# Performance work log

Hardware: AMD Instinct MI355X
Metric: run time of the kernel (lower is better)

## Reference

```python
import jax, jax.numpy as jnp
import numpy as np

N_ENT = 40000
D = 128
B = 1024
EPS = 1e-7  # BCE clamp for numerical stability (torch clamps logs internally)


def _cdist_euclidean(a, e):
    # a: [B, D], e: [N, D] -> [B, N] via GEMM-based squared-distance expansion
    sq = jnp.sum(a * a, axis=1)[:, None] + jnp.sum(e * e, axis=1)[None, :] - 2.0 * (a @ e.T)
    return jnp.sqrt(jnp.maximum(sq, 0.0))


def _cdist_manhattan(a, e):
    # Sequential over batch rows to avoid materializing [B, N, D]
    return jax.lax.map(lambda row: jnp.sum(jnp.abs(row[None, :] - e), axis=1), a)


def _branch_loss(c, ent, t_idx, l1_flag, positive):
    dist = _cdist_manhattan(c, ent) if l1_flag else _cdist_euclidean(c, ent)
    # original Python double-loop: dist[i][j] = 1/dist[i][j] * 100
    scaled = 100.0 / jnp.maximum(dist, 1e-12)
    pred = jnp.clip(jax.nn.sigmoid(scaled), EPS, 1.0 - EPS)
    if positive:
        y = jnp.zeros_like(pred).at[jnp.arange(pred.shape[0]), t_idx].set(1.0)
        bce = y * jnp.log(pred) + (1.0 - y) * jnp.log(1.0 - pred)
    else:
        # negative branch writes 0 into an all-zeros target -> y == 0
        bce = jnp.log(1.0 - pred)
    return -jnp.mean(bce)


def setup_inputs() -> dict:
    key = jax.random.key(0)
    ks = jax.random.split(key, 7)
    return {
        "pos_h_batch": jax.random.randint(ks[0], (B,), 0, N_ENT),
        "pos_t_batch": jax.random.randint(ks[1], (B,), 0, N_ENT),
        "neg_h_batch": jax.random.randint(ks[2], (B,), 0, N_ENT),
        "neg_t_batch": jax.random.randint(ks[3], (B,), 0, N_ENT),
        "rseq_pos": jax.random.normal(ks[4], (B, D), jnp.float32),
        "rseq_neg": jax.random.normal(ks[5], (B, D), jnp.float32),
        "ent_embeddings": jax.random.normal(ks[6], (N_ENT, D), jnp.float32),
        "L1_flag": 0,
    }


def reference(pos_h_batch, pos_t_batch, neg_h_batch, neg_t_batch, rseq_pos, rseq_neg, ent_embeddings, L1_flag):
    l1 = bool(L1_flag)
    # positive branch
    c_t_pos = ent_embeddings[pos_h_batch] + rseq_pos
    loss1 = _branch_loss(c_t_pos, ent_embeddings, pos_t_batch, l1, positive=True)
    # negative branch (neg_t_batch only feeds an unused c_h_e in the original)
    c_t_neg = ent_embeddings[neg_h_batch] + rseq_neg
    loss2 = _branch_loss(c_t_neg, ent_embeddings, None, l1, positive=False)
    return loss1 + loss2
```

## Files before the change

kernel.cpp:

```cpp
#include <hip/hip_runtime.h>
#include <cstdint>
#include <cstddef>

#define N_ENT 40000
#define DDIM  128
#define BSZ   1024
#define NJT   313
#define NPART (16 * NJT)
#define NGRID 5120

#define AS1 __attribute__((address_space(1)))
#define AS3 __attribute__((address_space(3)))

typedef short s16x8 __attribute__((ext_vector_type(8)));
typedef float f32x4 __attribute__((ext_vector_type(4)));

#define OFF_PART  0
#define OFF_TPART 20480
#define OFF_ENORM 24576
#define OFF_CNORM 184576
#define OFF_CBF   192768
#define OFF_EBF   717056

#define S_CLAMP 15.9423847f
#define U_CLAMP 0.159423847f
#define LP_MAX (-1.1920929e-7f)

__device__ __forceinline__ unsigned short f2bf(float f) {
  uint32_t u = __float_as_uint(f);
  u += 0x7fffu + ((u >> 16) & 1u);
  return (unsigned short)(u >> 16);
}

__global__ __launch_bounds__(256) void prep_k(const float* __restrict__ ent,
                                              const int* __restrict__ pos_h,
                                              const int* __restrict__ pos_t,
                                              const int* __restrict__ neg_h,
                                              const float* __restrict__ rpos,
                                              const float* __restrict__ rneg,
                                              const int* __restrict__ l1_flag,
                                              unsigned short* __restrict__ ent_bf,
                                              float* __restrict__ enorm,
                                              unsigned short* __restrict__ c_bf,
                                              float* __restrict__ cnorm,
                                              float* __restrict__ tpart) {
  const int lane = threadIdx.x & 63, wv = threadIdx.x >> 6;
  const int ih = lane >> 5, il = lane & 31;
  const int blk = blockIdx.x;
  if (blk < 5000) {
    int row = blk * 8 + wv * 2 + ih;
    float4 v = reinterpret_cast<const float4*>(ent + (size_t)row * DDIM)[il];
    ushort4 h4; h4.x = f2bf(v.x); h4.y = f2bf(v.y); h4.z = f2bf(v.z); h4.w = f2bf(v.w);
    reinterpret_cast<ushort4*>(ent_bf + (size_t)row * DDIM)[il] = h4;
    float sq = fmaf(v.x, v.x, fmaf(v.y, v.y, fmaf(v.z, v.z, v.w * v.w)));
    #pragma unroll
    for (int m = 1; m <= 16; m <<= 1) sq += __shfl_xor(sq, m);
    if (il == 0) enorm[row] = sq;
  } else {
    int row = (blk - 5000) * 8 + wv * 2 + ih;
    int br = row >> 10, i = row & 1023;
    int h = br ? neg_h[i] : pos_h[i];
    const float* rs = br ? rneg : rpos;
    float4 e  = reinterpret_cast<const float4*>(ent + (size_t)h * DDIM)[il];
    float4 rv = reinterpret_cast<const float4*>(rs + (size_t)i * DDIM)[il];
    float c0 = e.x + rv.x, c1 = e.y + rv.y, c2 = e.z + rv.z, c3 = e.w + rv.w;
    ushort4 h4; h4.x = f2bf(c0); h4.y = f2bf(c1); h4.z = f2bf(c2); h4.w = f2bf(c3);
    reinterpret_cast<ushort4*>(c_bf + (size_t)row * DDIM)[il] = h4;
    float sq = fmaf(c0, c0, fmaf(c1, c1, fmaf(c2, c2, c3 * c3)));
    #pragma unroll
    for (int m = 1; m <= 16; m <<= 1) sq += __shfl_xor(sq, m);
    if (il == 0) cnorm[row] = sq;
    if (br == 0) {
      int t = pos_t[i];
      float4 et = reinterpret_cast<const float4*>(ent + (size_t)t * DDIM)[il];
      float d0 = c0 - et.x, d1 = c1 - et.y, d2v = c2 - et.z, d3 = c3 - et.w;
      float d2 = fmaf(d0, d0, fmaf(d1, d1, fmaf(d2v, d2v, d3 * d3)));
      float m1 = fabsf(d0) + fabsf(d1) + fabsf(d2v) + fabsf(d3);
      #pragma unroll
      for (int m = 1; m <= 16; m <<= 1) { d2 += __shfl_xor(d2, m); m1 += __shfl_xor(m1, m); }
      if (il == 0) {
        float s = (*l1_flag) ? (100.f / fmaxf(m1, 1e-12f))
                             : (100.f * rsqrtf(fmaxf(d2, 0.f)));
        float x  = __expf(-s);
        float L  = log1pf(x);
        float Bt = fminf(-L, LP_MAX);
        float Ap = fmaxf(-s, -S_CLAMP);
        tpart[i] = Bt - Ap;
      }
    }
  }
}

__global__ __launch_bounds__(256) void main_k(const unsigned short* __restrict__ c_bf,
                                              const unsigned short* __restrict__ ent_bf,
                                              const float* __restrict__ cnorm,
                                              const float* __restrict__ enorm,
                                              const int* __restrict__ l1_flag,
                                              const int* __restrict__ pos_h,
                                              const int* __restrict__ neg_h,
                                              const float* __restrict__ rpos,
                                              const float* __restrict__ rneg,
                                              const float* __restrict__ ent_f32,
                                              float* __restrict__ partials) {
  __shared__ unsigned short smem[128 * 128];
  const int id = blockIdx.x;
  const int c8 = id & 7;
  const int q  = id >> 3;
  const int tg = q >> 4;
  const int mm = q & 15;
  const int jt = c8 + tg * 8;
  if (jt >= NJT) return;
  const int branch = mm & 1;
  const int it = mm >> 1;
  const int i0 = it * 128, j0 = jt * 128;
  const int tid = threadIdx.x, lane = tid & 63, wv = tid >> 6;
  const int wm = wv >> 1, wn = wv & 1;
  const int r15 = lane & 15, quad = lane >> 4;

  #pragma unroll
  for (int i = 0; i < 8; ++i) {
    int g  = i * 256 + tid;
    int r  = g >> 4;
    int cp = g & 15;
    int c  = cp ^ (r & 15);
    int jr = j0 + r; if (jr >= N_ENT) jr = N_ENT - 1;
    const unsigned short* src = ent_bf + (size_t)jr * DDIM + c * 8;
    __builtin_amdgcn_global_load_lds((const AS1 void*)src, (AS3 void*)(&smem[g * 8]), 16, 0, 0);
  }

  const unsigned short* Abase = c_bf + ((size_t)(branch << 10) + i0) * DDIM;
  const unsigned short* arow[4];
  #pragma unroll
  for (int tm = 0; tm < 4; ++tm)
    arow[tm] = Abase + (size_t)(wm * 64 + tm * 16 + r15) * DDIM + quad * 8;

  s16x8 av[2][4];
  #pragma unroll
  for (int tm = 0; tm < 4; ++tm)
    av[0][tm] = *reinterpret_cast<const s16x8*>(arow[tm]);

  float en[4];
  #pragma unroll
  for (int tn = 0; tn < 4; ++tn) {
    int jg = j0 + wn * 64 + tn * 16 + r15;
    en[tn] = enorm[jg < N_ENT ? jg : N_ENT - 1];
  }
  float cnv[16];
  #pragma unroll
  for (int tm = 0; tm < 4; ++tm)
    #pragma unroll
    for (int r = 0; r < 4; ++r)
      cnv[tm * 4 + r] = cnorm[(branch << 10) + i0 + wm * 64 + tm * 16 + quad * 4 + r];

  f32x4 acc[4][4];
  const f32x4 zf = {0.f, 0.f, 0.f, 0.f};
  #pragma unroll
  for (int a = 0; a < 4; ++a)
    #pragma unroll
    for (int b = 0; b < 4; ++b) acc[a][b] = zf;

  __syncthreads();

  #pragma unroll
  for (int kc = 0; kc < 4; ++kc) {
    if (kc < 3) {
      #pragma unroll
      for (int tm = 0; tm < 4; ++tm)
        av[(kc + 1) & 1][tm] = *reinterpret_cast<const s16x8*>(arow[tm] + (kc + 1) * 32);
    }
    s16x8 bv[4];
    #pragma unroll
    for (int tn = 0; tn < 4; ++tn) {
      int R  = wn * 64 + tn * 16 + r15;
      int cs = (kc * 4 + quad) ^ r15;
      bv[tn] = *reinterpret_cast<const s16x8*>(&smem[R * 128 + cs * 8]);
    }
    #pragma unroll
    for (int tm = 0; tm < 4; ++tm)
      #pragma unroll
      for (int tn = 0; tn < 4; ++tn)
        acc[tm][tn] = __builtin_amdgcn_mfma_f32_16x16x32_bf16(av[kc & 1][tm], bv[tn], acc[tm][tn], 0, 0, 0);
  }

  const int l1 = *l1_flag;
  float ls0 = 0.f, ls1 = 0.f, ls2 = 0.f, ls3 = 0.f;
  const bool full = (j0 + 128) <= N_ENT;

  if (!l1) {
    #pragma unroll
    for (int tm = 0; tm < 4; ++tm) {
      if (full) {
        #pragma unroll
        for (int tn = 0; tn < 4; ++tn) {
          float e0 = en[tn];
          float u0 = rsqrtf(fmaf(-2.f, acc[tm][tn][0], cnv[tm * 4 + 0] + e0));
          float u1 = rsqrtf(fmaf(-2.f, acc[tm][tn][1], cnv[tm * 4 + 1] + e0));
          float u2 = rsqrtf(fmaf(-2.f, acc[tm][tn][2], cnv[tm * 4 + 2] + e0));
          float u3 = rsqrtf(fmaf(-2.f, acc[tm][tn][3], cnv[tm * 4 + 3] + e0));
          ls0 += fminf(u0, U_CLAMP);
          ls1 += fminf(u1, U_CLAMP);
          ls2 += fminf(u2, U_CLAMP);
          ls3 += fminf(u3, U_CLAMP);
        }
      } else {
        #pragma unroll
        for (int tn = 0; tn < 4; ++tn) {
          int jg = j0 + wn * 64 + tn * 16 + r15;
          if (jg < N_ENT) {
            float e0 = en[tn];
            ls0 += fminf(rsqrtf(fmaf(-2.f, acc[tm][tn][0], cnv[tm * 4 + 0] + e0)), U_CLAMP);
            ls1 += fminf(rsqrtf(fmaf(-2.f, acc[tm][tn][1], cnv[tm * 4 + 1] + e0)), U_CLAMP);
            ls2 += fminf(rsqrtf(fmaf(-2.f, acc[tm][tn][2], cnv[tm * 4 + 2] + e0)), U_CLAMP);
            ls3 += fminf(rsqrtf(fmaf(-2.f, acc[tm][tn][3], cnv[tm * 4 + 3] + e0)), U_CLAMP);
          }
        }
      }
    }
  } else {
    const float* rs = branch ? rneg : rpos;
    const int*   hb = branch ? neg_h : pos_h;
    #pragma unroll 1
    for (int tm = 0; tm < 4; ++tm) {
      #pragma unroll 1
      for (int r = 0; r < 4; ++r) {
        int bi = i0 + wm * 64 + tm * 16 + quad * 4 + r;
        int h  = hb[bi];
        #pragma unroll 1
        for (int tn = 0; tn < 4; ++tn) {
          int jg = j0 + wn * 64 + tn * 16 + r15;
          if (jg < N_ENT) {
            const float* cp1 = ent_f32 + (size_t)h * DDIM;
            const float* cp2 = rs + (size_t)bi * DDIM;
            const float* ep  = ent_f32 + (size_t)jg * DDIM;
            float man = 0.f;
            #pragma unroll 1
            for (int d = 0; d < DDIM; ++d) man += fabsf(cp1[d] + cp2[d] - ep[d]);
            float s = 100.f / fmaxf(man, 1e-12f);
            ls0 += 0.01f * fminf(s, S_CLAMP);
          }
        }
      }
    }
  }
  float lsum = (ls0 + ls1) + (ls2 + ls3);

  #pragma unroll
  for (int m = 32; m; m >>= 1) lsum += __shfl_xor(lsum, m);
  __shared__ float s4[4];
  if (lane == 0) s4[wv] = lsum;
  __syncthreads();
  if (tid == 0)
    partials[jt * 16 + mm] = s4[0] + s4[1] + s4[2] + s4[3];
}

__global__ __launch_bounds__(256) void finalize_k(const float* __restrict__ partials,
                                                  const float* __restrict__ tpart,
                                                  float* __restrict__ out) {
  const int b = blockIdx.x, tid = threadIdx.x, lane = tid & 63, wv = tid >> 6;
  const double inv = 1.0 / ((double)BSZ * (double)N_ENT);
  double v = 0.0;
  if (b < 20) {
    int i = b * 256 + tid;
    if (i < NPART) v = (double)partials[i] * (100.0 * inv);
  } else {
    int i = (b - 20) * 256 + tid;
    v = (double)tpart[i] * (-inv);
  }
  #pragma unroll
  for (int m = 32; m; m >>= 1) v += __shfl_xor(v, m);
  __shared__ double sd[4];
  if (lane == 0) sd[wv] = v;
  __syncthreads();
  if (tid == 0) atomicAdd(out, (float)(sd[0] + sd[1] + sd[2] + sd[3]));
}

extern "C" void kernel_launch(void* const* d_in, const int* in_sizes, int n_in,
                              void* d_out, int out_size, void* d_ws, size_t ws_size,
                              hipStream_t stream) {
  const int*   pos_h = (const int*)d_in[0];
  const int*   pos_t = (const int*)d_in[1];
  const int*   neg_h = (const int*)d_in[2];
  const float* rpos  = (const float*)d_in[4];
  const float* rneg  = (const float*)d_in[5];
  const float* ent   = (const float*)d_in[6];
  const int*   l1    = (const int*)d_in[7];

  char* ws = (char*)d_ws;
  float*          partials = (float*)(ws + OFF_PART);
  float*          tpart    = (float*)(ws + OFF_TPART);
  float*          enorm    = (float*)(ws + OFF_ENORM);
  float*          cnorm    = (float*)(ws + OFF_CNORM);
  unsigned short* c_bf     = (unsigned short*)(ws + OFF_CBF);
  unsigned short* ent_bf   = (unsigned short*)(ws + OFF_EBF);

  hipMemsetAsync(d_out, 0, sizeof(float), stream);

  prep_k<<<5256, 256, 0, stream>>>(ent, pos_h, pos_t, neg_h, rpos, rneg, l1,
                                   ent_bf, enorm, c_bf, cnorm, tpart);

  main_k<<<NGRID, 256, 0, stream>>>(c_bf, ent_bf, cnorm, enorm, l1,
                                    pos_h, neg_h, rpos, rneg, ent, partials);

  finalize_k<<<24, 256, 0, stream>>>(partials, tpart, (float*)d_out);
}
```

Measured before the change: 144.2 us.

## Reuse each staged entity tile across four row tiles per block and single-block finalize

Each main_k block now loads one 128-entity bf16 tile into LDS once and loops over four consecutive row tiles (branch/i0 pairs), cutting the grid from 5120 to 1280 blocks and reducing redundant LDS staging of the entity tile by 4x. The next row tile's A fragments and norms are prefetched while the current tile's epilogue runs. The finalize kernel becomes a single 1024-thread block that writes the output directly, removing the memset and the atomics. The trade-off is fewer blocks available to hide latency and a serialized inner loop per block.

```diff
diff --git a/kernel.cpp b/kernel.cpp
--- a/kernel.cpp
+++ b/kernel.cpp
@@ -7,7 +7,7 @@
 #define BSZ   1024
 #define NJT   313
 #define NPART (16 * NJT)
-#define NGRID 5120
+#define NGRID 1280
 
 #define AS1 __attribute__((address_space(1)))
 #define AS3 __attribute__((address_space(3)))
@@ -103,16 +103,15 @@
                                               const float* __restrict__ ent_f32,
                                               float* __restrict__ partials) {
   __shared__ unsigned short smem[128 * 128];
+  __shared__ float s4[4][4];
   const int id = blockIdx.x;
   const int c8 = id & 7;
   const int q  = id >> 3;
-  const int tg = q >> 4;
-  const int mm = q & 15;
+  const int tg = q >> 2;
+  const int h  = q & 3;
   const int jt = c8 + tg * 8;
   if (jt >= NJT) return;
-  const int branch = mm & 1;
-  const int it = mm >> 1;
-  const int i0 = it * 128, j0 = jt * 128;
+  const int j0 = jt * 128;
   const int tid = threadIdx.x, lane = tid & 63, wv = tid >> 6;
   const int wm = wv >> 1, wn = wv & 1;
   const int r15 = lane & 15, quad = lane >> 4;
@@ -128,16 +127,31 @@
     __builtin_amdgcn_global_load_lds((const AS1 void*)src, (AS3 void*)(&smem[g * 8]), 16, 0, 0);
   }
 
-  const unsigned short* Abase = c_bf + ((size_t)(branch << 10) + i0) * DDIM;
+#define SET_AROW(mm_) do {                                                     \
+    int b_ = (mm_) & 1, i0_ = ((mm_) >> 1) * 128;                              \
+    const unsigned short* Ab = c_bf + ((size_t)(b_ << 10) + i0_) * DDIM;       \
+    _Pragma("unroll")                                                          \
+    for (int tm = 0; tm < 4; ++tm)                                             \
+      arow[tm] = Ab + (size_t)(wm * 64 + tm * 16 + r15) * DDIM + quad * 8;     \
+  } while (0)
+
+#define LOAD_CNV(mm_) do {                                                     \
+    int b_ = (mm_) & 1, i0_ = ((mm_) >> 1) * 128;                              \
+    _Pragma("unroll")                                                          \
+    for (int tm = 0; tm < 4; ++tm)                                             \
+      _Pragma("unroll")                                                        \
+      for (int r = 0; r < 4; ++r)                                              \
+        cnvA[tm * 4 + r] = cnorm[(b_ << 10) + i0_ + wm * 64 + tm * 16 + quad * 4 + r]; \
+  } while (0)
+
   const unsigned short* arow[4];
-  #pragma unroll
-  for (int tm = 0; tm < 4; ++tm)
-    arow[tm] = Abase + (size_t)(wm * 64 + tm * 16 + r15) * DDIM + quad * 8;
-
   s16x8 av[2][4];
+  float cnvA[16];
+  SET_AROW(h * 4);
   #pragma unroll
   for (int tm = 0; tm < 4; ++tm)
     av[0][tm] = *reinterpret_cast<const s16x8*>(arow[tm]);
+  LOAD_CNV(h * 4);
 
   float en[4];
   #pragma unroll
@@ -145,133 +159,145 @@
     int jg = j0 + wn * 64 + tn * 16 + r15;
     en[tn] = enorm[jg < N_ENT ? jg : N_ENT - 1];
   }
-  float cnv[16];
-  #pragma unroll
-  for (int tm = 0; tm < 4; ++tm)
-    #pragma unroll
-    for (int r = 0; r < 4; ++r)
-      cnv[tm * 4 + r] = cnorm[(branch << 10) + i0 + wm * 64 + tm * 16 + quad * 4 + r];
-
-  f32x4 acc[4][4];
+
+  const int l1 = *l1_flag;
+  const bool full = (j0 + 128) <= N_ENT;
   const f32x4 zf = {0.f, 0.f, 0.f, 0.f};
-  #pragma unroll
-  for (int a = 0; a < 4; ++a)
-    #pragma unroll
-    for (int b = 0; b < 4; ++b) acc[a][b] = zf;
 
   __syncthreads();
 
-  #pragma unroll
-  for (int kc = 0; kc < 4; ++kc) {
-    if (kc < 3) {
+  #pragma unroll 1
+  for (int k = 0; k < 4; ++k) {
+    const int mm = h * 4 + k;
+    const int branch = mm & 1;
+    const int i0 = (mm >> 1) * 128;
+
+    f32x4 acc[4][4];
+    #pragma unroll
+    for (int a = 0; a < 4; ++a)
+      #pragma unroll
+      for (int b = 0; b < 4; ++b) acc[a][b] = zf;
+
+    #pragma unroll
+    for (int kc = 0; kc < 4; ++kc) {
+      if (kc < 3) {
+        #pragma unroll
+        for (int tm = 0; tm < 4; ++tm)
+          av[(kc + 1) & 1][tm] = *reinterpret_cast<const s16x8*>(arow[tm] + (kc + 1) * 32);
+      }
+      s16x8 bv[4];
+      #pragma unroll
+      for (int tn = 0; tn < 4; ++tn) {
+        int R  = wn * 64 + tn * 16 + r15;
+        int cs = (kc * 4 + quad) ^ r15;
+        bv[tn] = *reinterpret_cast<const s16x8*>(&smem[R * 128 + cs * 8]);
+      }
       #pragma unroll
       for (int tm = 0; tm < 4; ++tm)
-        av[(kc + 1) & 1][tm] = *reinterpret_cast<const s16x8*>(arow[tm] + (kc + 1) * 32);
+        #pragma unroll
+        for (int tn = 0; tn < 4; ++tn)
+          acc[tm][tn] = __builtin_amdgcn_mfma_f32_16x16x32_bf16(av[kc & 1][tm], bv[tn], acc[tm][tn], 0, 0, 0);
     }
-    s16x8 bv[4];
-    #pragma unroll
-    for (int tn = 0; tn < 4; ++tn) {
-      int R  = wn * 64 + tn * 16 + r15;
-      int cs = (kc * 4 + quad) ^ r15;
-      bv[tn] = *reinterpret_cast<const s16x8*>(&smem[R * 128 + cs * 8]);
+
+    if (k < 3) {
+      SET_AROW(mm + 1);
+      #pragma unroll
+      for (int tm = 0; tm < 4; ++tm)
+        av[0][tm] = *reinterpret_cast<const s16x8*>(arow[tm]);
     }
-    #pragma unroll
-    for (int tm = 0; tm < 4; ++tm)
-      #pragma unroll
-      for (int tn = 0; tn < 4; ++tn)
-        acc[tm][tn] = __builtin_amdgcn_mfma_f32_16x16x32_bf16(av[kc & 1][tm], bv[tn], acc[tm][tn], 0, 0, 0);
-  }
-
-  const int l1 = *l1_flag;
-  float ls0 = 0.f, ls1 = 0.f, ls2 = 0.f, ls3 = 0.f;
-  const bool full = (j0 + 128) <= N_ENT;
-
-  if (!l1) {
-    #pragma unroll
-    for (int tm = 0; tm < 4; ++tm) {
-      if (full) {
-        #pragma unroll
-        for (int tn = 0; tn < 4; ++tn) {
-          float e0 = en[tn];
-          float u0 = rsqrtf(fmaf(-2.f, acc[tm][tn][0], cnv[tm * 4 + 0] + e0));
-          float u1 = rsqrtf(fmaf(-2.f, acc[tm][tn][1], cnv[tm * 4 + 1] + e0));
-          float u2 = rsqrtf(fmaf(-2.f, acc[tm][tn][2], cnv[tm * 4 + 2] + e0));
-          float u3 = rsqrtf(fmaf(-2.f, acc[tm][tn][3], cnv[tm * 4 + 3] + e0));
-          ls0 += fminf(u0, U_CLAMP);
-          ls1 += fminf(u1, U_CLAMP);
-          ls2 += fminf(u2, U_CLAMP);
-          ls3 += fminf(u3, U_CLAMP);
-        }
-      } else {
-        #pragma unroll
-        for (int tn = 0; tn < 4; ++tn) {
-          int jg = j0 + wn * 64 + tn * 16 + r15;
-          if (jg < N_ENT) {
+
+    float ls0 = 0.f, ls1 = 0.f, ls2 = 0.f, ls3 = 0.f;
+    if (!l1) {
+      #pragma unroll
+      for (int tm = 0; tm < 4; ++tm) {
+        if (full) {
+          #pragma unroll
+          for (int tn = 0; tn < 4; ++tn) {
             float e0 = en[tn];
-            ls0 += fminf(rsqrtf(fmaf(-2.f, acc[tm][tn][0], cnv[tm * 4 + 0] + e0)), U_CLAMP);
-            ls1 += fminf(rsqrtf(fmaf(-2.f, acc[tm][tn][1], cnv[tm * 4 + 1] + e0)), U_CLAMP);
-            ls2 += fminf(rsqrtf(fmaf(-2.f, acc[tm][tn][2], cnv[tm * 4 + 2] + e0)), U_CLAMP);
-            ls3 += fminf(rsqrtf(fmaf(-2.f, acc[tm][tn][3], cnv[tm * 4 + 3] + e0)), U_CLAMP);
+            float u0 = rsqrtf(fmaf(-2.f, acc[tm][tn][0], cnvA[tm * 4 + 0] + e0));
+            float u1 = rsqrtf(fmaf(-2.f, acc[tm][tn][1], cnvA[tm * 4 + 1] + e0));
+            float u2 = rsqrtf(fmaf(-2.f, acc[tm][tn][2], cnvA[tm * 4 + 2] + e0));
+            float u3 = rsqrtf(fmaf(-2.f, acc[tm][tn][3], cnvA[tm * 4 + 3] + e0));
+            ls0 += fminf(u0, U_CLAMP);
+            ls1 += fminf(u1, U_CLAMP);
+            ls2 += fminf(u2, U_CLAMP);
+            ls3 += fminf(u3, U_CLAMP);
+          }
+        } else {
+          #pragma unroll
+          for (int tn = 0; tn < 4; ++tn) {
+            int jg = j0 + wn * 64 + tn * 16 + r15;
+            if (jg < N_ENT) {
+              float e0 = en[tn];
+              ls0 += fminf(rsqrtf(fmaf(-2.f, acc[tm][tn][0], cnvA[tm * 4 + 0] + e0)), U_CLAMP);
+              ls1 += fminf(rsqrtf(fmaf(-2.f, acc[tm][tn][1], cnvA[tm * 4 + 1] + e0)), U_CLAMP);
+              ls2 += fminf(rsqrtf(fmaf(-2.f, acc[tm][tn][2], cnvA[tm * 4 + 2] + e0)), U_CLAMP);
+              ls3 += fminf(rsqrtf(fmaf(-2.f, acc[tm][tn][3], cnvA[tm * 4 + 3] + e0)), U_CLAMP);
+            }
           }
         }
       }
-    }
-  } else {
-    const float* rs = branch ? rneg : rpos;
-    const int*   hb = branch ? neg_h : pos_h;
-    #pragma unroll 1
-    for (int tm = 0; tm < 4; ++tm) {
+    } else {
+      const float* rs = branch ? rneg : rpos;
+      const int*   hb = branch ? neg_h : pos_h;
       #pragma unroll 1
-      for (int r = 0; r < 4; ++r) {
-        int bi = i0 + wm * 64 + tm * 16 + quad * 4 + r;
-        int h  = hb[bi];
+      for (int tm = 0; tm < 4; ++tm) {
         #pragma unroll 1
-        for (int tn = 0; tn < 4; ++tn) {
-          int jg = j0 + wn * 64 + tn * 16 + r15;
-          if (jg < N_ENT) {
-            const float* cp1 = ent_f32 + (size_t)h * DDIM;
-            const float* cp2 = rs + (size_t)bi * DDIM;
-            const float* ep  = ent_f32 + (size_t)jg * DDIM;
-            float man = 0.f;
-            #pragma unroll 1
-            for (int d = 0; d < DDIM; ++d) man += fabsf(cp1[d] + cp2[d] - ep[d]);
-            float s = 100.f / fmaxf(man, 1e-12f);
-            ls0 += 0.01f * fminf(s, S_CLAMP);
+        for (int r = 0; r < 4; ++r) {
+          int bi = i0 + wm * 64 + tm * 16 + quad * 4 + r;
+          int hh = hb[bi];
+          #pragma unroll 1
+          for (int tn = 0; tn < 4; ++tn) {
+            int jg = j0 + wn * 64 + tn * 16 + r15;
+            if (jg < N_ENT) {
+              const float* cp1 = ent_f32 + (size_t)hh * DDIM;
+              const float* cp2 = rs + (size_t)bi * DDIM;
+              const float* ep  = ent_f32 + (size_t)jg * DDIM;
+              float man = 0.f;
+              #pragma unroll 1
+              for (int d = 0; d < DDIM; ++d) man += fabsf(cp1[d] + cp2[d] - ep[d]);
+              float s = 100.f / fmaxf(man, 1e-12f);
+              ls0 += 0.01f * fminf(s, S_CLAMP);
+            }
           }
         }
       }
     }
-  }
-  float lsum = (ls0 + ls1) + (ls2 + ls3);
-
-  #pragma unroll
-  for (int m = 32; m; m >>= 1) lsum += __shfl_xor(lsum, m);
-  __shared__ float s4[4];
-  if (lane == 0) s4[wv] = lsum;
+    float lsum = (ls0 + ls1) + (ls2 + ls3);
+
+    #pragma unroll
+    for (int m = 32; m; m >>= 1) lsum += __shfl_xor(lsum, m);
+    if (lane == 0) s4[k][wv] = lsum;
+
+    if (k < 3) LOAD_CNV(mm + 1);
+  }
+
   __syncthreads();
-  if (tid == 0)
-    partials[jt * 16 + mm] = s4[0] + s4[1] + s4[2] + s4[3];
-}
-
-__global__ __launch_bounds__(256) void finalize_k(const float* __restrict__ partials,
-                                                  const float* __restrict__ tpart,
-                                                  float* __restrict__ out) {
-  const int b = blockIdx.x, tid = threadIdx.x, lane = tid & 63, wv = tid >> 6;
+  if (tid < 4)
+    partials[jt * 16 + h * 4 + tid] = s4[tid][0] + s4[tid][1] + s4[tid][2] + s4[tid][3];
+#undef SET_AROW
+#undef LOAD_CNV
+}
+
+__global__ __launch_bounds__(1024) void finalize_k(const float* __restrict__ partials,
+                                                   const float* __restrict__ tpart,
+                                                   float* __restrict__ out) {
+  const int tid = threadIdx.x, lane = tid & 63, wv = tid >> 6;
   const double inv = 1.0 / ((double)BSZ * (double)N_ENT);
   double v = 0.0;
-  if (b < 20) {
-    int i = b * 256 + tid;
-    if (i < NPART) v = (double)partials[i] * (100.0 * inv);
-  } else {
-    int i = (b - 20) * 256 + tid;
-    v = (double)tpart[i] * (-inv);
-  }
+  for (int i = tid; i < NPART; i += 1024) v += (double)partials[i] * (100.0 * inv);
+  v += (double)tpart[tid] * (-inv);
   #pragma unroll
   for (int m = 32; m; m >>= 1) v += __shfl_xor(v, m);
-  __shared__ double sd[4];
+  __shared__ double sd[16];
   if (lane == 0) sd[wv] = v;
   __syncthreads();
-  if (tid == 0) atomicAdd(out, (float)(sd[0] + sd[1] + sd[2] + sd[3]));
+  if (wv == 0) {
+    double t = (lane < 16) ? sd[lane] : 0.0;
+    #pragma unroll
+    for (int m = 8; m; m >>= 1) t += __shfl_xor(t, m);
+    if (lane == 0) out[0] = (float)t;
+  }
 }
 
 extern "C" void kernel_launch(void* const* d_in, const int* in_sizes, int n_in,
@@ -293,13 +319,11 @@
   unsigned short* c_bf     = (unsigned short*)(ws + OFF_CBF);
   unsigned short* ent_bf   = (unsigned short*)(ws + OFF_EBF);
 
-  hipMemsetAsync(d_out, 0, sizeof(float), stream);
-
   prep_k<<<5256, 256, 0, stream>>>(ent, pos_h, pos_t, neg_h, rpos, rneg, l1,
                                    ent_bf, enorm, c_bf, cnorm, tpart);
 
   main_k<<<NGRID, 256, 0, stream>>>(c_bf, ent_bf, cnorm, enorm, l1,
                                     pos_h, neg_h, rpos, rneg, ent, partials);
 
-  finalize_k<<<24, 256, 0, stream>>>(partials, tpart, (float*)d_out);
-}
+  finalize_k<<<1, 1024, 0, stream>>>(partials, tpart, (float*)d_out);
+}
```

After: 162.2 us. +12.4%, slower.

## Make main kernel persistent over column-tile chunks with double-buffered LDS staging

Applied to the files above, without the earlier changes.

Each block now handles up to five consecutive entity tiles instead of one. It keeps the A fragments and row norms in registers across tiles and double-buffers the entity tile in LDS, so the next tile's global-to-LDS load overlaps the current MFMA and epilogue work. The grid shrinks from 5120 blocks to 1024. The finalize step becomes a single 1024-thread block that writes the output directly, which removes the memset and the atomics. The cost is higher LDS and register use per block (two 32KB buffers) and fewer blocks to spread across CUs.

```diff
diff --git a/kernel.cpp b/kernel.cpp
--- a/kernel.cpp
+++ b/kernel.cpp
@@ -7,7 +7,8 @@
 #define BSZ   1024
 #define NJT   313
 #define NPART (16 * NJT)
-#define NGRID 5120
+#define CH    5
+#define NGRID 1024
 
 #define AS1 __attribute__((address_space(1)))
 #define AS3 __attribute__((address_space(3)))
@@ -91,187 +92,213 @@
   }
 }
 
-__global__ __launch_bounds__(256) void main_k(const unsigned short* __restrict__ c_bf,
-                                              const unsigned short* __restrict__ ent_bf,
-                                              const float* __restrict__ cnorm,
-                                              const float* __restrict__ enorm,
-                                              const int* __restrict__ l1_flag,
-                                              const int* __restrict__ pos_h,
-                                              const int* __restrict__ neg_h,
-                                              const float* __restrict__ rpos,
-                                              const float* __restrict__ rneg,
-                                              const float* __restrict__ ent_f32,
-                                              float* __restrict__ partials) {
-  __shared__ unsigned short smem[128 * 128];
+__global__ __launch_bounds__(256, 2) void main_k(const unsigned short* __restrict__ c_bf,
+                                                 const unsigned short* __restrict__ ent_bf,
+                                                 const float* __restrict__ cnorm,
+                                                 const float* __restrict__ enorm,
+                                                 const int* __restrict__ l1_flag,
+                                                 const int* __restrict__ pos_h,
+                                                 const int* __restrict__ neg_h,
+                                                 const float* __restrict__ rpos,
+                                                 const float* __restrict__ rneg,
+                                                 const float* __restrict__ ent_f32,
+                                                 float* __restrict__ partials) {
+  __shared__ unsigned short smem[2][128 * 128];
+  __shared__ float s4[2][4];
   const int id = blockIdx.x;
   const int c8 = id & 7;
   const int q  = id >> 3;
-  const int tg = q >> 4;
   const int mm = q & 15;
-  const int jt = c8 + tg * 8;
-  if (jt >= NJT) return;
+  const int gg = q >> 4;
+  const int gp = c8 * 8 + gg;
+  const int jtB = gp * CH;
+  if (jtB >= NJT) return;
+  const int nt = (jtB + CH <= NJT) ? CH : (NJT - jtB);
   const int branch = mm & 1;
-  const int it = mm >> 1;
-  const int i0 = it * 128, j0 = jt * 128;
+  const int i0 = (mm >> 1) * 128;
   const int tid = threadIdx.x, lane = tid & 63, wv = tid >> 6;
   const int wm = wv >> 1, wn = wv & 1;
   const int r15 = lane & 15, quad = lane >> 4;
 
+#define STAGE(par_, j0_) do {                                                  \
+    _Pragma("unroll")                                                          \
+    for (int i_ = 0; i_ < 8; ++i_) {                                           \
+      int g_  = i_ * 256 + tid;          \
+      int r_  = g_ >> 4;                                                       \
+      int c_  = (g_ & 15) ^ (r_ & 15);                                         \
+      int jr_ = (j0_) + r_; if (jr_ >= N_ENT) jr_ = N_ENT - 1;                 \
+      const unsigned short* src_ = ent_bf + (size_t)jr_ * DDIM + c_ * 8;       \
+      __builtin_amdgcn_global_load_lds((const AS1 void*)src_,                  \
+          (AS3 void*)(&smem[par_][g_ * 8]), 16, 0, 0);                         \
+    }                                                                          \
+  } while (0)
+
+  STAGE(0, jtB * 128);
+
+  const unsigned short* Abase = c_bf + ((size_t)(branch << 10) + i0) * DDIM;
+  s16x8 avk[4][4];
   #pragma unroll
-  for (int i = 0; i < 8; ++i) {
-    int g  = i * 256 + tid;
-    int r  = g >> 4;
-    int cp = g & 15;
-    int c  = cp ^ (r & 15);
-    int jr = j0 + r; if (jr >= N_ENT) jr = N_ENT - 1;
-    const unsigned short* src = ent_bf + (size_t)jr * DDIM + c * 8;
-    __builtin_amdgcn_global_load_lds((const AS1 void*)src, (AS3 void*)(&smem[g * 8]), 16, 0, 0);
-  }
-
-  const unsigned short* Abase = c_bf + ((size_t)(branch << 10) + i0) * DDIM;
-  const unsigned short* arow[4];
+  for (int tm = 0; tm < 4; ++tm) {
+    const unsigned short* ar = Abase + (size_t)(wm * 64 + tm * 16 + r15) * DDIM + quad * 8;
+    #pragma unroll
+    for (int kc = 0; kc < 4; ++kc)
+      avk[kc][tm] = *reinterpret_cast<const s16x8*>(ar + kc * 32);
+  }
+
+  float cnv[16];
   #pragma unroll
   for (int tm = 0; tm < 4; ++tm)
-    arow[tm] = Abase + (size_t)(wm * 64 + tm * 16 + r15) * DDIM + quad * 8;
-
-  s16x8 av[2][4];
-  #pragma unroll
-  for (int tm = 0; tm < 4; ++tm)
-    av[0][tm] = *reinterpret_cast<const s16x8*>(arow[tm]);
+    #pragma unroll
+    for (int r = 0; r < 4; ++r)
+      cnv[tm * 4 + r] = cnorm[(branch << 10) + i0 + wm * 64 + tm * 16 + quad * 4 + r];
 
   float en[4];
   #pragma unroll
   for (int tn = 0; tn < 4; ++tn) {
-    int jg = j0 + wn * 64 + tn * 16 + r15;
+    int jg = jtB * 128 + wn * 64 + tn * 16 + r15;
     en[tn] = enorm[jg < N_ENT ? jg : N_ENT - 1];
   }
-  float cnv[16];
-  #pragma unroll
-  for (int tm = 0; tm < 4; ++tm)
-    #pragma unroll
-    for (int r = 0; r < 4; ++r)
-      cnv[tm * 4 + r] = cnorm[(branch << 10) + i0 + wm * 64 + tm * 16 + quad * 4 + r];
-
-  f32x4 acc[4][4];
+
+  const int l1 = *l1_flag;
   const f32x4 zf = {0.f, 0.f, 0.f, 0.f};
-  #pragma unroll
-  for (int a = 0; a < 4; ++a)
-    #pragma unroll
-    for (int b = 0; b < 4; ++b) acc[a][b] = zf;
 
   __syncthreads();
 
-  #pragma unroll
-  for (int kc = 0; kc < 4; ++kc) {
-    if (kc < 3) {
+  #pragma unroll 1
+  for (int t = 0; t < nt; ++t) {
+    const int jt  = jtB + t;
+    const int j0  = jt * 128;
+    const int par = t & 1;
+    const bool haveNext = (t + 1) < nt;
+
+    if (haveNext) STAGE(par ^ 1, j0 + 128);
+
+    float enx[4];
+    if (haveNext) {
+      #pragma unroll
+      for (int tn = 0; tn < 4; ++tn) {
+        int jg = j0 + 128 + wn * 64 + tn * 16 + r15;
+        enx[tn] = enorm[jg < N_ENT ? jg : N_ENT - 1];
+      }
+    }
+
+    f32x4 acc[4][4];
+    #pragma unroll
+    for (int a = 0; a < 4; ++a)
+      #pragma unroll
+      for (int b = 0; b < 4; ++b) acc[a][b] = zf;
+
+    #pragma unroll
+    for (int kc = 0; kc < 4; ++kc) {
+      s16x8 bv[4];
+      #pragma unroll
+      for (int tn = 0; tn < 4; ++tn) {
+        int R  = wn * 64 + tn * 16 + r15;
+        int cs = (kc * 4 + quad) ^ r15;
+        bv[tn] = *reinterpret_cast<const s16x8*>(&smem[par][R * 128 + cs * 8]);
+      }
       #pragma unroll
       for (int tm = 0; tm < 4; ++tm)
-        av[(kc + 1) & 1][tm] = *reinterpret_cast<const s16x8*>(arow[tm] + (kc + 1) * 32);
-    }
-    s16x8 bv[4];
-    #pragma unroll
-    for (int tn = 0; tn < 4; ++tn) {
-      int R  = wn * 64 + tn * 16 + r15;
-      int cs = (kc * 4 + quad) ^ r15;
-      bv[tn] = *reinterpret_cast<const s16x8*>(&smem[R * 128 + cs * 8]);
-    }
-    #pragma unroll
-    for (int tm = 0; tm < 4; ++tm)
-      #pragma unroll
-      for (int tn = 0; tn < 4; ++tn)
-        acc[tm][tn] = __builtin_amdgcn_mfma_f32_16x16x32_bf16(av[kc & 1][tm], bv[tn], acc[tm][tn], 0, 0, 0);
-  }
-
-  const int l1 = *l1_flag;
-  float ls0 = 0.f, ls1 = 0.f, ls2 = 0.f, ls3 = 0.f;
-  const bool full = (j0 + 128) <= N_ENT;
-
-  if (!l1) {
-    #pragma unroll
-    for (int tm = 0; tm < 4; ++tm) {
-      if (full) {
         #pragma unroll
-        for (int tn = 0; tn < 4; ++tn) {
-          float e0 = en[tn];
-          float u0 = rsqrtf(fmaf(-2.f, acc[tm][tn][0], cnv[tm * 4 + 0] + e0));
-          float u1 = rsqrtf(fmaf(-2.f, acc[tm][tn][1], cnv[tm * 4 + 1] + e0));
-          float u2 = rsqrtf(fmaf(-2.f, acc[tm][tn][2], cnv[tm * 4 + 2] + e0));
-          float u3 = rsqrtf(fmaf(-2.f, acc[tm][tn][3], cnv[tm * 4 + 3] + e0));
-          ls0 += fminf(u0, U_CLAMP);
-          ls1 += fminf(u1, U_CLAMP);
-          ls2 += fminf(u2, U_CLAMP);
-          ls3 += fminf(u3, U_CLAMP);
-        }
-      } else {
-        #pragma unroll
-        for (int tn = 0; tn < 4; ++tn) {
-          int jg = j0 + wn * 64 + tn * 16 + r15;
-          if (jg < N_ENT) {
+        for (int tn = 0; tn < 4; ++tn)
+          acc[tm][tn] = __builtin_amdgcn_mfma_f32_16x16x32_bf16(avk[kc][tm], bv[tn], acc[tm][tn], 0, 0, 0);
+    }
+
+    const bool full = (j0 + 128) <= N_ENT;
+    float ls0 = 0.f, ls1 = 0.f, ls2 = 0.f, ls3 = 0.f;
+    if (!l1) {
+      #pragma unroll
+      for (int tm = 0; tm < 4; ++tm) {
+        if (full) {
+          #pragma unroll
+          for (int tn = 0; tn < 4; ++tn) {
             float e0 = en[tn];
-            ls0 += fminf(rsqrtf(fmaf(-2.f, acc[tm][tn][0], cnv[tm * 4 + 0] + e0)), U_CLAMP);
-            ls1 += fminf(rsqrtf(fmaf(-2.f, acc[tm][tn][1], cnv[tm * 4 + 1] + e0)), U_CLAMP);
-            ls2 += fminf(rsqrtf(fmaf(-2.f, acc[tm][tn][2], cnv[tm * 4 + 2] + e0)), U_CLAMP);
-            ls3 += fminf(rsqrtf(fmaf(-2.f, acc[tm][tn][3], cnv[tm * 4 + 3] + e0)), U_CLAMP);
+            float u0 = rsqrtf(fmaf(-2.f, acc[tm][tn][0], cnv[tm * 4 + 0] + e0));
+            float u1 = rsqrtf(fmaf(-2.f, acc[tm][tn][1], cnv[tm * 4 + 1] + e0));
+            float u2 = rsqrtf(fmaf(-2.f, acc[tm][tn][2], cnv[tm * 4 + 2] + e0));
+            float u3 = rsqrtf(fmaf(-2.f, acc[tm][tn][3], cnv[tm * 4 + 3] + e0));
+            ls0 += fminf(u0, U_CLAMP);
+            ls1 += fminf(u1, U_CLAMP);
+            ls2 += fminf(u2, U_CLAMP);
+            ls3 += fminf(u3, U_CLAMP);
+          }
+        } else {
+          #pragma unroll
+          for (int tn = 0; tn < 4; ++tn) {
+            int jg = j0 + wn * 64 + tn * 16 + r15;
+            if (jg < N_ENT) {
+              float e0 = en[tn];
+              ls0 += fminf(rsqrtf(fmaf(-2.f, acc[tm][tn][0], cnv[tm * 4 + 0] + e0)), U_CLAMP);
+              ls1 += fminf(rsqrtf(fmaf(-2.f, acc[tm][tn][1], cnv[tm * 4 + 1] + e0)), U_CLAMP);
+              ls2 += fminf(rsqrtf(fmaf(-2.f, acc[tm][tn][2], cnv[tm * 4 + 2] + e0)), U_CLAMP);
+              ls3 += fminf(rsqrtf(fmaf(-2.f, acc[tm][tn][3], cnv[tm * 4 + 3] + e0)), U_CLAMP);
+            }
           }
         }
       }
-    }
-  } else {
-    const float* rs = branch ? rneg : rpos;
-    const int*   hb = branch ? neg_h : pos_h;
-    #pragma unroll 1
-    for (int tm = 0; tm < 4; ++tm) {
+    } else {
+      const float* rs = branch ? rneg : rpos;
+      const int*   hb = branch ? neg_h : pos_h;
       #pragma unroll 1
-      for (int r = 0; r < 4; ++r) {
-        int bi = i0 + wm * 64 + tm * 16 + quad * 4 + r;
-        int h  = hb[bi];
+      for (int tm = 0; tm < 4; ++tm) {
         #pragma unroll 1
-        for (int tn = 0; tn < 4; ++tn) {
-          int jg = j0 + wn * 64 + tn * 16 + r15;
-          if (jg < N_ENT) {
-            const float* cp1 = ent_f32 + (size_t)h * DDIM;
-            const float* cp2 = rs + (size_t)bi * DDIM;
-            const float* ep  = ent_f32 + (size_t)jg * DDIM;
-            float man = 0.f;
-            #pragma unroll 1
-            for (int d = 0; d < DDIM; ++d) man += fabsf(cp1[d] + cp2[d] - ep[d]);
-            float s = 100.f / fmaxf(man, 1e-12f);
-            ls0 += 0.01f * fminf(s, S_CLAMP);
+        for (int r = 0; r < 4; ++r) {
+          int bi = i0 + wm * 64 + tm * 16 + quad * 4 + r;
+          int hh = hb[bi];
+          #pragma unroll 1
+          for (int tn = 0; tn < 4; ++tn) {
+            int jg = j0 + wn * 64 + tn * 16 + r15;
+            if (jg < N_ENT) {
+              const float* cp1 = ent_f32 + (size_t)hh * DDIM;
+              const float* cp2 = rs + (size_t)bi * DDIM;
+              const float* ep  = ent_f32 + (size_t)jg * DDIM;
+              float man = 0.f;
+              #pragma unroll 1
+              for (int d = 0; d < DDIM; ++d) man += fabsf(cp1[d] + cp2[d] - ep[d]);
+              float s = 100.f / fmaxf(man, 1e-12f);
+              ls0 += 0.01f * fminf(s, S_CLAMP);
+            }
           }
         }
       }
     }
-  }
-  float lsum = (ls0 + ls1) + (ls2 + ls3);
-
-  #pragma unroll
-  for (int m = 32; m; m >>= 1) lsum += __shfl_xor(lsum, m);
-  __shared__ float s4[4];
-  if (lane == 0) s4[wv] = lsum;
-  __syncthreads();
-  if (tid == 0)
-    partials[jt * 16 + mm] = s4[0] + s4[1] + s4[2] + s4[3];
-}
-
-__global__ __launch_bounds__(256) void finalize_k(const float* __restrict__ partials,
-                                                  const float* __restrict__ tpart,
-                                                  float* __restrict__ out) {
-  const int b = blockIdx.x, tid = threadIdx.x, lane = tid & 63, wv = tid >> 6;
+    float lsum = (ls0 + ls1) + (ls2 + ls3);
+
+    #pragma unroll
+    for (int m = 32; m; m >>= 1) lsum += __shfl_xor(lsum, m);
+    if (lane == 0) s4[par][wv] = lsum;
+
+    if (haveNext) {
+      #pragma unroll
+      for (int tn = 0; tn < 4; ++tn) en[tn] = enx[tn];
+    }
+
+    __syncthreads();
+    if (tid == 0)
+      partials[jt * 16 + mm] = s4[par][0] + s4[par][1] + s4[par][2] + s4[par][3];
+  }
+#undef STAGE
+}
+
+__global__ __launch_bounds__(1024) void finalize_k(const float* __restrict__ partials,
+                                                   const float* __restrict__ tpart,
+                                                   float* __restrict__ out) {
+  const int tid = threadIdx.x, lane = tid & 63, wv = tid >> 6;
   const double inv = 1.0 / ((double)BSZ * (double)N_ENT);
   double v = 0.0;
-  if (b < 20) {
-    int i = b * 256 + tid;
-    if (i < NPART) v = (double)partials[i] * (100.0 * inv);
-  } else {
-    int i = (b - 20) * 256 + tid;
-    v = (double)tpart[i] * (-inv);
-  }
+  for (int i = tid; i < NPART; i += 1024) v += (double)partials[i] * (100.0 * inv);
+  v += (double)tpart[tid] * (-inv);
   #pragma unroll
   for (int m = 32; m; m >>= 1) v += __shfl_xor(v, m);
-  __shared__ double sd[4];
+  __shared__ double sd[16];
   if (lane == 0) sd[wv] = v;
   __syncthreads();
-  if (tid == 0) atomicAdd(out, (float)(sd[0] + sd[1] + sd[2] + sd[3]));
+  if (wv == 0) {
+    double t = (lane < 16) ? sd[lane] : 0.0;
+    #pragma unroll
+    for (int m = 8; m; m >>= 1) t += __shfl_xor(t, m);
+    if (lane == 0) out[0] = (float)t;
+  }
 }
 
 extern "C" void kernel_launch(void* const* d_in, const int* in_sizes, int n_in,
@@ -293,13 +320,11 @@
   unsigned short* c_bf     = (unsigned short*)(ws + OFF_CBF);
   unsigned short* ent_bf   = (unsigned short*)(ws + OFF_EBF);
 
-  hipMemsetAsync(d_out, 0, sizeof(float), stream);
-
   prep_k<<<5256, 256, 0, stream>>>(ent, pos_h, pos_t, neg_h, rpos, rneg, l1,
                                    ent_bf, enorm, c_bf, cnorm, tpart);
 
   main_k<<<NGRID, 256, 0, stream>>>(c_bf, ent_bf, cnorm, enorm, l1,
                                     pos_h, neg_h, rpos, rneg, ent, partials);
 
-  finalize_k<<<24, 256, 0, stream>>>(partials, tpart, (float*)d_out);
-}
+  finalize_k<<<1, 1024, 0, stream>>>(partials, tpart, (float*)d_out);
+}
```

New measurement: 133.8 us. -7.2%, faster.
